# Optimization experiments

Measured on AMD Instinct MI355X. Metric: run time of the kernel, lower is better.

Reference implementation:

```python
import jax, jax.numpy as jnp
import numpy as np

B, T = 64, 128
IN, H, L, OUT = 512, 1024, 2, 1


def _gru_scan(seq, Wi, Wh, bi, bh):
    # seq: (S, in_dim); PyTorch GRU cell, gate order r, z, n.
    h0 = jnp.zeros((H,), dtype=seq.dtype)
    def step(h, x):
        gi = x @ Wi.T + bi          # (3H,)
        gh = h @ Wh.T + bh          # (3H,)
        r = jax.nn.sigmoid(gi[:H] + gh[:H])
        z = jax.nn.sigmoid(gi[H:2 * H] + gh[H:2 * H])
        n = jnp.tanh(gi[2 * H:] + r * gh[2 * H:])
        h_new = (1.0 - z) * n + z * h
        return h_new, h_new
    _, hs = jax.lax.scan(step, h0, seq)
    return hs                        # (S, H)


def setup_inputs() -> dict:
    key = jax.random.key(0)
    ks = jax.random.split(key, 24)
    mk = lambda k, shape: jax.random.normal(k, shape, dtype=jnp.float32) * 0.05
    d = {}
    d['x'] = jax.random.normal(ks[0], (B, T, IN), dtype=jnp.float32)
    # gru1: layer0 input=IN, layer1 input=H
    d['g1_Wi0'] = mk(ks[1], (3 * H, IN)); d['g1_Wh0'] = mk(ks[2], (3 * H, H))
    d['g1_bi0'] = mk(ks[3], (3 * H,));    d['g1_bh0'] = mk(ks[4], (3 * H,))
    d['g1_Wi1'] = mk(ks[5], (3 * H, H));  d['g1_Wh1'] = mk(ks[6], (3 * H, H))
    d['g1_bi1'] = mk(ks[7], (3 * H,));    d['g1_bh1'] = mk(ks[8], (3 * H,))
    # gru2: both layers input=H
    d['g2_Wi0'] = mk(ks[9], (3 * H, H));  d['g2_Wh0'] = mk(ks[10], (3 * H, H))
    d['g2_bi0'] = mk(ks[11], (3 * H,));   d['g2_bh0'] = mk(ks[12], (3 * H,))
    d['g2_Wi1'] = mk(ks[13], (3 * H, H)); d['g2_Wh1'] = mk(ks[14], (3 * H, H))
    d['g2_bi1'] = mk(ks[15], (3 * H,));   d['g2_bh1'] = mk(ks[16], (3 * H,))
    d['fc1_W'] = mk(ks[17], (64, H));     d['fc1_b'] = mk(ks[18], (64,))
    d['fc2_W'] = mk(ks[19], (OUT, 64));   d['fc2_b'] = mk(ks[20], (OUT,))
    return d


def reference(x, g1_Wi0, g1_Wh0, g1_bi0, g1_bh0, g1_Wi1, g1_Wh1, g1_bi1, g1_bh1,
              g2_Wi0, g2_Wh0, g2_bi0, g2_bh0, g2_Wi1, g2_Wh1, g2_bi1, g2_bh1,
              fc1_W, fc1_b, fc2_W, fc2_b):
    # PyTorch feeds x[:, t, :] (2-D) to a batch_first GRU -> treated as an
    # UNBATCHED sequence of length B; hidden is carried across t. That equals
    # one GRU scan over the flattened (T*B)-step sequence, t-major / b-minor.
    seq = jnp.swapaxes(x, 0, 1).reshape(T * B, IN)
    hs0 = _gru_scan(seq, g1_Wi0, g1_Wh0, g1_bi0, g1_bh0)    # (T*B, H) layer 0
    hs1 = _gru_scan(hs0, g1_Wi1, g1_Wh1, g1_bi1, g1_bh1)    # (T*B, H) layer 1
    # h returned after timestep t is the hidden at flat step t*B + (B-1)
    s = jnp.stack([hs0, hs1], axis=1)[B - 1::B]             # (T, L, H)
    seq2 = s.reshape(T * L, H)                              # torch.cat(s)
    # gru2 over the [1, T*L, H] sequence (batch=1)
    hs2_0 = _gru_scan(seq2, g2_Wi0, g2_Wh0, g2_bi0, g2_bh0)
    hs2_1 = _gru_scan(hs2_0, g2_Wi1, g2_Wh1, g2_bi1, g2_bh1)
    h2 = jnp.stack([hs2_0[-1], hs2_1[-1]], axis=0)[:, None, :]  # (L, 1, H)
    y = jax.nn.sigmoid(h2 @ fc1_W.T + fc1_b)                # (L, 1, 64)
    out = jax.nn.sigmoid(y @ fc2_W.T + fc2_b)               # (L, 1, OUT)
    return out
```

## Files before the change

### kernel.cpp

```cpp
#include <hip/hip_runtime.h>


typedef unsigned u32x4 __attribute__((ext_vector_type(4)));
typedef unsigned u32x2 __attribute__((ext_vector_type(2)));
typedef _Float16 h2_t  __attribute__((ext_vector_type(2)));

#define NWG 256

__device__ u32x4    g_recL0[2][NWG];
__device__ u32x4    g_recL1[2][NWG];
__device__ unsigned g_seq2[256][512];

__device__ __forceinline__ unsigned pk(float a, float b) {
  unsigned short ua = __builtin_bit_cast(unsigned short, (_Float16)a);
  unsigned short ub = __builtin_bit_cast(unsigned short, (_Float16)b);
  return (unsigned)ua | ((unsigned)ub << 16);
}
__device__ __forceinline__ float unpk(unsigned u, int hi) {
  unsigned short us = (unsigned short)(hi ? (u >> 16) : (u & 0xffffu));
  return (float)__builtin_bit_cast(_Float16, us);
}

#if __has_builtin(__builtin_amdgcn_fdot2)
__device__ __forceinline__ float fdot2(unsigned a, unsigned b, float c) {
  return __builtin_amdgcn_fdot2(__builtin_bit_cast(h2_t, a),
                                __builtin_bit_cast(h2_t, b), c, false);
}
#else
__device__ __forceinline__ float fdot2(unsigned a, unsigned b, float c) {
  h2_t ha = __builtin_bit_cast(h2_t, a), hb = __builtin_bit_cast(h2_t, b);
  return c + (float)ha[0] * (float)hb[0] + (float)ha[1] * (float)hb[1];
}
#endif

__device__ __forceinline__ u32x4 ld_sc_v4(const u32x4* p) {
  u32x4 v;
  asm volatile("global_load_dwordx4 %0, %1, off sc1\n\t"
               "s_waitcnt vmcnt(0)"
               : "=&v"(v) : "v"(p) : "memory");
  return v;
}
__device__ __forceinline__ void st_sc_v4(u32x4* p, u32x4 v) {
  asm volatile("global_store_dwordx4 %0, %1, off sc1"
               :: "v"(p), "v"(v) : "memory");
}
__device__ __forceinline__ void st_sc_v2(void* p, u32x2 v) {
  asm volatile("global_store_dwordx2 %0, %1, off sc1"
               :: "v"(p), "v"(v) : "memory");
}

__device__ __forceinline__ float rcpf(float x) {
#if __has_builtin(__builtin_amdgcn_rcpf)
  return __builtin_amdgcn_rcpf(x);
#else
  return 1.f / x;
#endif
}
__device__ __forceinline__ float sigf(float x) {
  return rcpf(1.f + __expf(-x));
}
__device__ __forceinline__ float tanh_f(float x) {
  x = fminf(fmaxf(x, -15.f), 15.f);
  const float e = __expf(2.f * x);
  return (e - 1.f) * rcpf(e + 1.f);
}

__device__ __forceinline__ int swzHc(int ch) { return ch ^ ((ch >> 3) & 7); }
__device__ __forceinline__ int swzXc(int ch) { return ch ^ ((ch >> 2) & 7); }
__device__ __forceinline__ int swzH_pos(int idx) { return (swzHc(idx >> 2) << 2) | (idx & 3); }
__device__ __forceinline__ int swzX_pos(int idx) { return (swzXc(idx >> 2) << 2) | (idx & 3); }

__global__ void init_recs() {
  int t = blockIdx.x * blockDim.x + threadIdx.x;
  u32x4 ff = {0u, 0u, 0xFFFFFFFFu, 0u};
  if (t < 512)       g_recL0[t >> 8][t & 255] = ff;
  else               g_recL1[(t - 512) >> 8][t & 255] = ff;
}

template <int PHASE>
__global__ __launch_bounds__(512, 2) void gru_phase(
    const float* __restrict__ Wm0, const float* __restrict__ Wm1,
    const float* __restrict__ Wm2, const float* __restrict__ Wm3,
    const float* __restrict__ bh0, const float* __restrict__ bi1,
    const float* __restrict__ bh1, const float* __restrict__ bi0,
    const float* __restrict__ x,
    const float* __restrict__ fc1W, const float* __restrict__ fc1b,
    const float* __restrict__ fc2W, const float* __restrict__ fc2b,
    float* __restrict__ out)
{
  constexpr int N0 = (PHASE == 1) ? 8192 : 256;
  constexpr int XC = (PHASE == 1) ? 512 : 1024;

  const int wg   = blockIdx.x;
  const int tid  = threadIdx.x;
  const int wv   = tid >> 6;
  const int lane = tid & 63;
  const int m    = wv >> 1;
  const int kh   = wv & 1;
  const int g4   = lane >> 4;
  const int q    = lane & 15;
  const int j0   = wg * 4;
  const bool m3s = (PHASE == 1) && (m == 3);

  __shared__ __attribute__((aligned(16))) unsigned sH0[2][512];
  __shared__ __attribute__((aligned(16))) unsigned sH1[2][512];
  __shared__ __attribute__((aligned(16))) unsigned sX [2][512];
  __shared__ float sD[2][96];
  __shared__ float sY[128];

  unsigned wreg[48];
  {
    const float* Wm = (m == 0) ? Wm0 : (m == 1) ? Wm1 : (m == 2) ? Wm2 : Wm3;
    const int cols = (m == 3) ? XC : 1024;
    #pragma unroll
    for (int t = 0; t < 3; ++t) {
      const int rr = g4 * 3 + t;
      const int R  = (rr >> 2) * 1024 + j0 + (rr & 3);
      const float2* rp = (const float2*)(Wm + (size_t)R * cols + kh * (cols / 2) + q * (cols / 32));
      if (m3s) {
        #pragma unroll
        for (int p = 0; p < 8; ++p)  { float2 v = rp[p]; wreg[t * 8 + p]  = pk(v.x, v.y); }
      } else {
        #pragma unroll
        for (int p = 0; p < 16; ++p) { float2 v = rp[p]; wreg[t * 16 + p] = pk(v.x, v.y); }
      }
    }
  }

  float bI[3], bH[3];
  {
    const int i = lane & 3, layer = (lane >> 2) & 1;
    const float* pbi = layer ? bi1 : bi0;
    const float* pbh = layer ? bh1 : bh0;
    #pragma unroll
    for (int g = 0; g < 3; ++g) {
      bI[g] = pbi[g * 1024 + j0 + i];
      bH[g] = pbh[g * 1024 + j0 + i];
    }
  }

  for (int s = 0; s <= N0; ++s) {
    const int par = s & 1;

    float2 xv = {0.f, 0.f};
    unsigned xs = 0;
    if (PHASE == 1) {
      if (s < N0 && tid < 256) {
        const int b = s & 63, tt = s >> 6;
        xv = ((const float2*)(x + (size_t)(b * 128 + tt) * 512))[tid];
      }
    } else {
      if (s < N0) xs = g_seq2[s][tid];
    }

    const int t2 = tid & 255;
    {
      unsigned d0 = 0, d1 = 0;
      if (s > 0) {
        const unsigned want = (unsigned)(s - 1);
        const u32x4* a = (tid < 256) ? &g_recL0[(s - 1) & 1][t2]
                                     : &g_recL1[(s - 1) & 1][t2];
        u32x4 r = ld_sc_v4(a);
        while (r[2] != want) {
          __builtin_amdgcn_s_sleep(1);
          r = ld_sc_v4(a);
        }
        d0 = r[0]; d1 = r[1];
      }
      unsigned* dst = (tid < 256) ? sH0[par] : sH1[par];
      dst[swzH_pos(2 * t2)]     = d0;
      dst[swzH_pos(2 * t2 + 1)] = d1;
    }
    if (PHASE == 1) {
      if (s < N0 && tid < 256) sX[par][swzX_pos(tid)] = pk(xv.x, xv.y);
    } else {
      if (s < N0) sX[par][swzH_pos(tid)] = xs;
    }
    __syncthreads();

    float acc0 = 0.f, acc1 = 0.f, acc2 = 0.f;
    if (m3s) {
      const u32x4* Xv = (const u32x4*)sX[par];
      #pragma unroll
      for (int k = 0; k < 2; ++k) {
        u32x4 h4 = Xv[swzXc(kh * 32 + 2 * q + k)];
        #pragma unroll
        for (int u = 0; u < 4; ++u) {
          const int p = 4 * k + u;
          acc0 = fdot2(wreg[p],      h4[u], acc0);
          acc1 = fdot2(wreg[8 + p],  h4[u], acc1);
          acc2 = fdot2(wreg[16 + p], h4[u], acc2);
        }
      }
    } else {
      const unsigned* hb = (m == 2) ? sH1[par] : (m == 3) ? sX[par] : sH0[par];
      const u32x4* Hv = (const u32x4*)hb;
      #pragma unroll
      for (int k = 0; k < 4; ++k) {
        u32x4 h4 = Hv[swzHc(kh * 64 + 4 * q + k)];
        #pragma unroll
        for (int u = 0; u < 4; ++u) {
          const int p = 4 * k + u;
          acc0 = fdot2(wreg[p],      h4[u], acc0);
          acc1 = fdot2(wreg[16 + p], h4[u], acc1);
          acc2 = fdot2(wreg[32 + p], h4[u], acc2);
        }
      }
    }
    acc0 += __shfl_xor(acc0, 8, 16); acc0 += __shfl_xor(acc0, 4, 16);
    acc0 += __shfl_xor(acc0, 2, 16); acc0 += __shfl_xor(acc0, 1, 16);
    acc1 += __shfl_xor(acc1, 8, 16); acc1 += __shfl_xor(acc1, 4, 16);
    acc1 += __shfl_xor(acc1, 2, 16); acc1 += __shfl_xor(acc1, 1, 16);
    acc2 += __shfl_xor(acc2, 8, 16); acc2 += __shfl_xor(acc2, 4, 16);
    acc2 += __shfl_xor(acc2, 2, 16); acc2 += __shfl_xor(acc2, 1, 16);
    if (q < 3) {
      const float dv = (q == 0) ? acc0 : (q == 1) ? acc1 : acc2;
      sD[par][m * 24 + kh * 12 + g4 * 3 + q] = dv;
    }
    __syncthreads();

    if (wv == 0) {
      const int i = lane & 3;
      const int layer = (lane >> 2) & 1;
      const float* Sd = sD[par];
      const int mI = layer ? 1 : 3;
      const int mH = layer ? 2 : 0;
      const float dIr = Sd[mI * 24 + 0 + i] + Sd[mI * 24 + 12 + 0 + i];
      const float dIz = Sd[mI * 24 + 4 + i] + Sd[mI * 24 + 12 + 4 + i];
      const float dIn = Sd[mI * 24 + 8 + i] + Sd[mI * 24 + 12 + 8 + i];
      const float dHr = Sd[mH * 24 + 0 + i] + Sd[mH * 24 + 12 + 0 + i];
      const float dHz = Sd[mH * 24 + 4 + i] + Sd[mH * 24 + 12 + 4 + i];
      const float dHn = Sd[mH * 24 + 8 + i] + Sd[mH * 24 + 12 + 8 + i];
      const float rg = sigf(dIr + bI[0] + dHr + bH[0]);
      const float zg = sigf(dIz + bI[1] + dHz + bH[1]);
      const float ng = tanh_f(dIn + bI[2] + rg * (dHn + bH[2]));
      const int   jj = 2 * wg + (i >> 1);
      const unsigned hu = (layer ? sH1 : sH0)[par][swzH_pos(jj)];
      const float hp = unpk(hu, i & 1);
      float hn = (1.f - zg) * ng + zg * hp;
      const bool valid = layer ? (s >= 1) : (s < N0);
      hn = valid ? hn : 0.f;
      const float v0 = __shfl(hn, 0), v1 = __shfl(hn, 1);
      const float v2 = __shfl(hn, 2), v3 = __shfl(hn, 3);
      const float w0 = __shfl(hn, 4), w1 = __shfl(hn, 5);
      const float w2 = __shfl(hn, 6), w3 = __shfl(hn, 7);
      if (lane == 0) {
        u32x4 rec0 = {pk(v0, v1), pk(v2, v3), (unsigned)s, 0u};
        u32x4 rec1 = {pk(w0, w1), pk(w2, w3), (unsigned)s, 0u};
        st_sc_v4(&g_recL0[par][wg], rec0);
        st_sc_v4(&g_recL1[par][wg], rec1);
        if (PHASE == 1) {
          if ((s & 63) == 63) {
            u32x2 t2v = {rec0[0], rec0[1]};
            st_sc_v2(&g_seq2[2 * (s >> 6)][2 * wg], t2v);
          }
          if (s >= 1 && ((s - 1) & 63) == 63) {
            u32x2 t2v = {rec1[0], rec1[1]};
            st_sc_v2(&g_seq2[2 * ((s - 1) >> 6) + 1][2 * wg], t2v);
          }
        }
      }
    }
  }

  if (PHASE == 2 && wg == 0) {
    if (tid < 256) {
      const u32x4* a1 = &g_recL1[0][tid];
      u32x4 r1 = ld_sc_v4(a1);
      while (r1[2] != 256u) { __builtin_amdgcn_s_sleep(1); r1 = ld_sc_v4(a1); }
      sH1[0][swzH_pos(2 * tid)]     = r1[0];
      sH1[0][swzH_pos(2 * tid + 1)] = r1[1];
    }
    __syncthreads();
    if (tid < 128) {
      const int lsel = tid >> 6;
      const int k = tid & 63;
      const unsigned* Hs = lsel ? sH1[0] : sH0[0];
      const float* wrow = fc1W + (size_t)k * 1024;
      float a = fc1b[k];
      for (int j2 = 0; j2 < 512; ++j2) {
        const unsigned hu = Hs[swzH_pos(j2)];
        a += unpk(hu, 0) * wrow[2 * j2] + unpk(hu, 1) * wrow[2 * j2 + 1];
      }
      sY[tid] = sigf(a);
    }
    __syncthreads();
    if (tid < 2) {
      const float* yv = sY + tid * 64;
      float a = fc2b[0];
      for (int k2 = 0; k2 < 64; ++k2) a += fc2W[k2] * yv[k2];
      out[tid] = sigf(a);
    }
  }
}

extern "C" void kernel_launch(void* const* d_in, const int* in_sizes, int n_in,
                              void* d_out, int out_size, void* d_ws, size_t ws_size,
                              hipStream_t stream) {
  (void)in_sizes; (void)n_in; (void)out_size; (void)d_ws; (void)ws_size;
  const float* x      = (const float*)d_in[0];
  const float* g1_Wi0 = (const float*)d_in[1];
  const float* g1_Wh0 = (const float*)d_in[2];
  const float* g1_bi0 = (const float*)d_in[3];
  const float* g1_bh0 = (const float*)d_in[4];
  const float* g1_Wi1 = (const float*)d_in[5];
  const float* g1_Wh1 = (const float*)d_in[6];
  const float* g1_bi1 = (const float*)d_in[7];
  const float* g1_bh1 = (const float*)d_in[8];
  const float* g2_Wi0 = (const float*)d_in[9];
  const float* g2_Wh0 = (const float*)d_in[10];
  const float* g2_bi0 = (const float*)d_in[11];
  const float* g2_bh0 = (const float*)d_in[12];
  const float* g2_Wi1 = (const float*)d_in[13];
  const float* g2_Wh1 = (const float*)d_in[14];
  const float* g2_bi1 = (const float*)d_in[15];
  const float* g2_bh1 = (const float*)d_in[16];
  const float* fc1W   = (const float*)d_in[17];
  const float* fc1b   = (const float*)d_in[18];
  const float* fc2W   = (const float*)d_in[19];
  const float* fc2b   = (const float*)d_in[20];
  float* out = (float*)d_out;

  init_recs<<<dim3(4), dim3(256), 0, stream>>>();
  gru_phase<1><<<dim3(NWG), dim3(512), 0, stream>>>(
      g1_Wh0, g1_Wi1, g1_Wh1, g1_Wi0, g1_bh0, g1_bi1, g1_bh1, g1_bi0,
      x, fc1W, fc1b, fc2W, fc2b, out);
  gru_phase<2><<<dim3(NWG), dim3(512), 0, stream>>>(
      g2_Wh0, g2_Wi1, g2_Wh1, g2_Wi0, g2_bh0, g2_bi1, g2_bh1, g2_bi0,
      x, fc1W, fc1b, fc2W, fc2b, out);
}
```

Measured before the change: 26.79 ms.

## Pipeline all four GRU layers in one persistent kernel with per-XCC roles

Replaces the two-phase launch, where each phase ran its two layers in lockstep, with a single persistent kernel. Workgroups claim slots through atomics and become one of four layer roles, each role placed on its own XCC when possible, so all four GRU layers run as a wavefront pipeline. Each layer's hidden states are written to full per-step history buffers with sequence tags, letting downstream layers prefetch inputs several steps ahead. Pollers on the same XCC spin mostly through L2 loads. This removes the serialization between the two GRU stacks, but adds a large init pass over the history buffers, relies on XCC_ID placement, and needs every workgroup co-resident to avoid deadlock.

After: 25.51 ms. -4.8%, faster.

```diff
diff --git a/kernel.cpp b/kernel.cpp
--- a/kernel.cpp
+++ b/kernel.cpp
@@ -2,14 +2,16 @@
 
 
 typedef unsigned u32x4 __attribute__((ext_vector_type(4)));
-typedef unsigned u32x2 __attribute__((ext_vector_type(2)));
 typedef _Float16 h2_t  __attribute__((ext_vector_type(2)));
 
-#define NWG 256
-
-__device__ u32x4    g_recL0[2][NWG];
-__device__ u32x4    g_recL1[2][NWG];
-__device__ unsigned g_seq2[256][512];
+#define S1 8192
+#define S2 256
+
+__device__ u32x4 g_h0s[S1][256];
+__device__ u32x4 g_h1s[S1][256];
+__device__ u32x4 g_q0s[S2][256];
+__device__ u32x4 g_q1s[S2][256];
+__device__ int   g_claim[128];
 
 __device__ __forceinline__ unsigned pk(float a, float b) {
   unsigned short ua = __builtin_bit_cast(unsigned short, (_Float16)a);
@@ -36,17 +38,17 @@
 __device__ __forceinline__ u32x4 ld_sc_v4(const u32x4* p) {
   u32x4 v;
   asm volatile("global_load_dwordx4 %0, %1, off sc1\n\t"
-               "s_waitcnt vmcnt(0)"
-               : "=&v"(v) : "v"(p) : "memory");
+               "s_waitcnt vmcnt(0)" : "=&v"(v) : "v"(p) : "memory");
   return v;
 }
+__device__ __forceinline__ u32x4 ld_l2_v4(const u32x4* p) {
+  u32x4 v;
+  asm volatile("global_load_dwordx4 %0, %1, off sc0\n\t"
+               "s_waitcnt vmcnt(0)" : "=&v"(v) : "v"(p) : "memory");
+  return v;
+}
 __device__ __forceinline__ void st_sc_v4(u32x4* p, u32x4 v) {
-  asm volatile("global_store_dwordx4 %0, %1, off sc1"
-               :: "v"(p), "v"(v) : "memory");
-}
-__device__ __forceinline__ void st_sc_v2(void* p, u32x2 v) {
-  asm volatile("global_store_dwordx2 %0, %1, off sc1"
-               :: "v"(p), "v"(v) : "memory");
+  asm volatile("global_store_dwordx4 %0, %1, off sc1" :: "v"(p), "v"(v) : "memory");
 }
 
 __device__ __forceinline__ float rcpf(float x) {
@@ -56,9 +58,7 @@
   return 1.f / x;
 #endif
 }
-__device__ __forceinline__ float sigf(float x) {
-  return rcpf(1.f + __expf(-x));
-}
+__device__ __forceinline__ float sigf(float x) { return rcpf(1.f + __expf(-x)); }
 __device__ __forceinline__ float tanh_f(float x) {
   x = fminf(fmaxf(x, -15.f), 15.f);
   const float e = __expf(2.f * x);
@@ -66,230 +66,309 @@
 }
 
 __device__ __forceinline__ int swzHc(int ch) { return ch ^ ((ch >> 3) & 7); }
+__device__ __forceinline__ int swzH_pos(int i) { return (swzHc(i >> 2) << 2) | (i & 3); }
 __device__ __forceinline__ int swzXc(int ch) { return ch ^ ((ch >> 2) & 7); }
-__device__ __forceinline__ int swzH_pos(int idx) { return (swzHc(idx >> 2) << 2) | (idx & 3); }
-__device__ __forceinline__ int swzX_pos(int idx) { return (swzXc(idx >> 2) << 2) | (idx & 3); }
-
-__global__ void init_recs() {
-  int t = blockIdx.x * blockDim.x + threadIdx.x;
-  u32x4 ff = {0u, 0u, 0xFFFFFFFFu, 0u};
-  if (t < 512)       g_recL0[t >> 8][t & 255] = ff;
-  else               g_recL1[(t - 512) >> 8][t & 255] = ff;
-}
-
-template <int PHASE>
-__global__ __launch_bounds__(512, 2) void gru_phase(
-    const float* __restrict__ Wm0, const float* __restrict__ Wm1,
-    const float* __restrict__ Wm2, const float* __restrict__ Wm3,
-    const float* __restrict__ bh0, const float* __restrict__ bi1,
-    const float* __restrict__ bh1, const float* __restrict__ bi0,
-    const float* __restrict__ x,
-    const float* __restrict__ fc1W, const float* __restrict__ fc1b,
-    const float* __restrict__ fc2W, const float* __restrict__ fc2b,
-    float* __restrict__ out)
+__device__ __forceinline__ int swzX_pos(int i) { return (swzXc(i >> 2) << 2) | (i & 3); }
+
+__global__ void init_all() {
+  const long long NH = (long long)S1 * 256;
+  const long long NQ = (long long)S2 * 256;
+  const long long N  = 2 * NH + 2 * NQ;
+  for (long long k = (long long)blockIdx.x * blockDim.x + threadIdx.x; k < N;
+       k += (long long)gridDim.x * blockDim.x) {
+    u32x4* r;
+    long long k2 = k;
+    if (k2 < NH) r = &g_h0s[0][0] + k2;
+    else {
+      k2 -= NH;
+      if (k2 < NH) r = &g_h1s[0][0] + k2;
+      else {
+        k2 -= NH;
+        if (k2 < NQ) r = &g_q0s[0][0] + k2;
+        else         r = &g_q1s[0][0] + (k2 - NQ);
+      }
+    }
+    (*r)[2] = 0xFFFFFFFFu;
+  }
+  if (blockIdx.x == 0 && threadIdx.x < 128) g_claim[threadIdx.x] = 0;
+}
+
+__device__ __forceinline__ const u32x4* in_addr(int role, int u, int r) {
+  if (role == 1) return &g_h0s[u][r];
+  if (role == 2) {
+    const int ss = ((u >> 1) << 6) + 63;
+    return (u & 1) ? &g_h1s[ss][r] : &g_h0s[ss][r];
+  }
+  return &g_q0s[u][r];
+}
+__device__ __forceinline__ unsigned in_want(int role, int u) {
+  return (role == 2) ? (unsigned)(((u >> 1) << 6) + 63) : (unsigned)u;
+}
+
+#define MAC4(A, W4, H4)                                                       \
+  A = fdot2((W4)[0], (H4)[0], A); A = fdot2((W4)[1], (H4)[1], A);             \
+  A = fdot2((W4)[2], (H4)[2], A); A = fdot2((W4)[3], (H4)[3], A);
+
+#define RED16(A)                                                              \
+  A += __shfl_xor(A, 8, 16); A += __shfl_xor(A, 4, 16);                       \
+  A += __shfl_xor(A, 2, 16); A += __shfl_xor(A, 1, 16);
+
+__global__
+__attribute__((amdgpu_flat_work_group_size(512, 512), amdgpu_waves_per_eu(2, 2)))
+void gru_all(const float* __restrict__ x,
+             const float* __restrict__ g1_Wi0, const float* __restrict__ g1_Wh0,
+             const float* __restrict__ g1_bi0, const float* __restrict__ g1_bh0,
+             const float* __restrict__ g1_Wi1, const float* __restrict__ g1_Wh1,
+             const float* __restrict__ g1_bi1, const float* __restrict__ g1_bh1,
+             const float* __restrict__ g2_Wi0, const float* __restrict__ g2_Wh0,
+             const float* __restrict__ g2_bi0, const float* __restrict__ g2_bh0,
+             const float* __restrict__ g2_Wi1, const float* __restrict__ g2_Wh1,
+             const float* __restrict__ g2_bi1, const float* __restrict__ g2_bh1,
+             const float* __restrict__ fc1W, const float* __restrict__ fc1b,
+             const float* __restrict__ fc2W, const float* __restrict__ fc2b,
+             float* __restrict__ out)
 {
-  constexpr int N0 = (PHASE == 1) ? 8192 : 256;
-  constexpr int XC = (PHASE == 1) ? 512 : 1024;
-
-  const int wg   = blockIdx.x;
-  const int tid  = threadIdx.x;
-  const int wv   = tid >> 6;
-  const int lane = tid & 63;
-  const int m    = wv >> 1;
-  const int kh   = wv & 1;
-  const int g4   = lane >> 4;
-  const int q    = lane & 15;
-  const int j0   = wg * 4;
-  const bool m3s = (PHASE == 1) && (m == 3);
-
-  __shared__ __attribute__((aligned(16))) unsigned sH0[2][512];
-  __shared__ __attribute__((aligned(16))) unsigned sH1[2][512];
-  __shared__ __attribute__((aligned(16))) unsigned sX [2][512];
-  __shared__ float sD[2][96];
+  const int tid = threadIdx.x;
+  const int G   = tid >> 4;
+  const int q   = tid & 15;
+  const int rid = tid - 256;
+
+  __shared__ __attribute__((aligned(16))) unsigned sH[2][512];
+  __shared__ __attribute__((aligned(16))) unsigned sIN[8][512];
+  __shared__ __attribute__((aligned(16))) unsigned sX[8][256];
+  __shared__ float sD[96];
+  __shared__ float sDI[96];
   __shared__ float sY[128];
-
-  unsigned wreg[48];
+  __shared__ int   sSlot;
+
+  unsigned xcc;
+  asm volatile("s_getreg_b32 %0, hwreg(HW_REG_XCC_ID)" : "=s"(xcc));
+  xcc &= 7u;
+  if (tid == 0) {
+    int slot = -1;
+    if (xcc < 4u) {
+      for (int i = 0; i < 32 && slot < 0; ++i)
+        if (atomicCAS(&g_claim[(int)xcc * 32 + i], 0, 1) == 0)
+          slot = (int)xcc * 32 + i;
+    }
+    if (slot < 0) {
+      for (int k = 0; k < 32; ++k) __builtin_amdgcn_s_sleep(64);
+      for (int i = 0; i < 128 && slot < 0; ++i)
+        if (atomicCAS(&g_claim[i], 0, 1) == 0) slot = i;
+    }
+    sSlot = slot;
+  }
+  __syncthreads();
+  const int slot = sSlot;
+  if (slot < 0) return;
+  const int role = slot >> 5;
+  const int rank = slot & 31;
+  const int e0   = rank * 32;
+  const bool lp  = ((int)xcc == role);
+  const int S    = (role <= 1) ? S1 : S2;
+
+  const float* Wh  = (role == 0) ? g1_Wh0 : (role == 1) ? g1_Wh1
+                   : (role == 2) ? g2_Wh0 : g2_Wh1;
+  const float* Wi  = (role == 0) ? g1_Wi0 : (role == 1) ? g1_Wi1
+                   : (role == 2) ? g2_Wi0 : g2_Wi1;
+  const float* pbi = (role == 0) ? g1_bi0 : (role == 1) ? g1_bi1
+                   : (role == 2) ? g2_bi0 : g2_bi1;
+  const float* pbh = (role == 0) ? g1_bh0 : (role == 1) ? g1_bh1
+                   : (role == 2) ? g2_bh0 : g2_bh1;
+  u32x4 (*outA)[256] = (role == 0) ? g_h0s : (role == 1) ? g_h1s
+                     : (role == 2) ? g_q0s : g_q1s;
+
+  u32x4 wv[6][8];
   {
-    const float* Wm = (m == 0) ? Wm0 : (m == 1) ? Wm1 : (m == 2) ? Wm2 : Wm3;
-    const int cols = (m == 3) ? XC : 1024;
+    const bool isWh = (G < 16);
+    const int  Gm   = isWh ? G : (G - 16);
+    const float* M  = isWh ? Wh : Wi;
+    const bool wide = isWh || (role != 0);
     #pragma unroll
-    for (int t = 0; t < 3; ++t) {
-      const int rr = g4 * 3 + t;
-      const int R  = (rr >> 2) * 1024 + j0 + (rr & 3);
-      const float2* rp = (const float2*)(Wm + (size_t)R * cols + kh * (cols / 2) + q * (cols / 32));
-      if (m3s) {
+    for (int j = 0; j < 6; ++j) {
+      const int rr = Gm * 6 + j;
+      const int R  = (rr >> 5) * 1024 + e0 + (rr & 31);
+      if (wide) {
+        const float4* rp = (const float4*)(M + (size_t)R * 1024 + 64 * q);
         #pragma unroll
-        for (int p = 0; p < 8; ++p)  { float2 v = rp[p]; wreg[t * 8 + p]  = pk(v.x, v.y); }
+        for (int c = 0; c < 8; ++c) {
+          float4 a = rp[2 * c], b = rp[2 * c + 1];
+          wv[j][c] = (u32x4){pk(a.x, a.y), pk(a.z, a.w), pk(b.x, b.y), pk(b.z, b.w)};
+        }
+      } else {
+        const float4* rp = (const float4*)(M + (size_t)R * 512 + 32 * q);
+        #pragma unroll
+        for (int c = 0; c < 4; ++c) {
+          float4 a = rp[2 * c], b = rp[2 * c + 1];
+          wv[j][c] = (u32x4){pk(a.x, a.y), pk(a.z, a.w), pk(b.x, b.y), pk(b.z, b.w)};
+        }
+      }
+    }
+  }
+
+  float bIr = 0, bIz = 0, bIn = 0, bHr = 0, bHz = 0, bHn = 0;
+  if (tid < 32) {
+    const int ge = e0 + tid;
+    bIr = pbi[ge]; bIz = pbi[1024 + ge]; bIn = pbi[2048 + ge];
+    bHr = pbh[ge]; bHz = pbh[1024 + ge]; bHn = pbh[2048 + ge];
+  }
+
+  if (tid >= 256) {
+    if (role == 0) {
+      #pragma unroll
+      for (int u = 0; u < 4; ++u) {
+        float2 xv = ((const float2*)(x + (size_t)((u & 63) * 128 + (u >> 6)) * 512))[rid];
+        sX[u][swzX_pos(rid)] = pk(xv.x, xv.y);
+      }
+    } else {
+      for (int u = 0; u < 4; ++u) {
+        const u32x4* a = in_addr(role, u, rid);
+        const unsigned w = in_want(role, u);
+        u32x4 r = ld_sc_v4(a);
+        while (r[2] != w) r = ld_sc_v4(a);
+        sIN[u][swzH_pos(2 * rid)]     = r[0];
+        sIN[u][swzH_pos(2 * rid + 1)] = r[1];
+      }
+    }
+  }
+  __syncthreads();
+
+  for (int s = 0; s < S; ++s) {
+    const int par = s & 1;
+
+    if (tid >= 256 && (s & 3) == 0) {
+      if (role == 0) {
+        #pragma unroll
+        for (int k = 0; k < 4; ++k) {
+          const int u = s + 4 + k;
+          if (u < S) {
+            float2 xv = ((const float2*)(x + (size_t)((u & 63) * 128 + (u >> 6)) * 512))[rid];
+            sX[u & 7][swzX_pos(rid)] = pk(xv.x, xv.y);
+          }
+        }
       } else {
         #pragma unroll
-        for (int p = 0; p < 16; ++p) { float2 v = rp[p]; wreg[t * 16 + p] = pk(v.x, v.y); }
-      }
-    }
-  }
-
-  float bI[3], bH[3];
-  {
-    const int i = lane & 3, layer = (lane >> 2) & 1;
-    const float* pbi = layer ? bi1 : bi0;
-    const float* pbh = layer ? bh1 : bh0;
-    #pragma unroll
-    for (int g = 0; g < 3; ++g) {
-      bI[g] = pbi[g * 1024 + j0 + i];
-      bH[g] = pbh[g * 1024 + j0 + i];
-    }
-  }
-
-  for (int s = 0; s <= N0; ++s) {
-    const int par = s & 1;
-
-    float2 xv = {0.f, 0.f};
-    unsigned xs = 0;
-    if (PHASE == 1) {
-      if (s < N0 && tid < 256) {
-        const int b = s & 63, tt = s >> 6;
-        xv = ((const float2*)(x + (size_t)(b * 128 + tt) * 512))[tid];
-      }
-    } else {
-      if (s < N0) xs = g_seq2[s][tid];
-    }
-
-    const int t2 = tid & 255;
-    {
+        for (int k = 0; k < 4; ++k) {
+          const int u = s + 4 + k;
+          if (u < S) {
+            const u32x4* a = in_addr(role, u, rid);
+            const unsigned w = in_want(role, u);
+            u32x4 r = ld_sc_v4(a);
+            while (r[2] != w) r = ld_sc_v4(a);
+            sIN[u & 7][swzH_pos(2 * rid)]     = r[0];
+            sIN[u & 7][swzH_pos(2 * rid + 1)] = r[1];
+          }
+        }
+      }
+    }
+
+    if (tid < 256) {
       unsigned d0 = 0, d1 = 0;
       if (s > 0) {
-        const unsigned want = (unsigned)(s - 1);
-        const u32x4* a = (tid < 256) ? &g_recL0[(s - 1) & 1][t2]
-                                     : &g_recL1[(s - 1) & 1][t2];
-        u32x4 r = ld_sc_v4(a);
-        while (r[2] != want) {
-          __builtin_amdgcn_s_sleep(1);
+        const unsigned w = (unsigned)(s - 1);
+        const u32x4* a = &outA[s - 1][tid];
+        u32x4 r;
+        if (lp) {
+          r = ld_l2_v4(a);
+          int spin = 0;
+          while (r[2] != w)
+            r = (((++spin) & 7) == 0) ? ld_sc_v4(a) : ld_l2_v4(a);
+        } else {
           r = ld_sc_v4(a);
+          while (r[2] != w) r = ld_sc_v4(a);
         }
         d0 = r[0]; d1 = r[1];
       }
-      unsigned* dst = (tid < 256) ? sH0[par] : sH1[par];
-      dst[swzH_pos(2 * t2)]     = d0;
-      dst[swzH_pos(2 * t2 + 1)] = d1;
-    }
-    if (PHASE == 1) {
-      if (s < N0 && tid < 256) sX[par][swzX_pos(tid)] = pk(xv.x, xv.y);
+      sH[par][swzH_pos(2 * tid)]     = d0;
+      sH[par][swzH_pos(2 * tid + 1)] = d1;
+    }
+    __syncthreads();
+
+    float a0 = 0, a1 = 0, a2 = 0, a3 = 0, a4 = 0, a5 = 0;
+    if (G < 16) {
+      const u32x4* HV = (const u32x4*)sH[par];
+      #pragma unroll
+      for (int c = 0; c < 8; ++c) {
+        const u32x4 h4 = HV[8 * q + (c ^ (q & 7))];
+        MAC4(a0, wv[0][c], h4); MAC4(a1, wv[1][c], h4); MAC4(a2, wv[2][c], h4);
+        MAC4(a3, wv[3][c], h4); MAC4(a4, wv[4][c], h4); MAC4(a5, wv[5][c], h4);
+      }
+    } else if (role != 0) {
+      const u32x4* IV = (const u32x4*)sIN[s & 7];
+      #pragma unroll
+      for (int c = 0; c < 8; ++c) {
+        const u32x4 h4 = IV[8 * q + (c ^ (q & 7))];
+        MAC4(a0, wv[0][c], h4); MAC4(a1, wv[1][c], h4); MAC4(a2, wv[2][c], h4);
+        MAC4(a3, wv[3][c], h4); MAC4(a4, wv[4][c], h4); MAC4(a5, wv[5][c], h4);
+      }
     } else {
-      if (s < N0) sX[par][swzH_pos(tid)] = xs;
+      const u32x4* XV = (const u32x4*)sX[s & 7];
+      #pragma unroll
+      for (int c = 0; c < 4; ++c) {
+        const int ch = 4 * q + c;
+        const u32x4 h4 = XV[ch ^ ((ch >> 2) & 7)];
+        MAC4(a0, wv[0][c], h4); MAC4(a1, wv[1][c], h4); MAC4(a2, wv[2][c], h4);
+        MAC4(a3, wv[3][c], h4); MAC4(a4, wv[4][c], h4); MAC4(a5, wv[5][c], h4);
+      }
+    }
+    RED16(a0); RED16(a1); RED16(a2); RED16(a3); RED16(a4); RED16(a5);
+    if (q < 6) {
+      const float v = (q == 0) ? a0 : (q == 1) ? a1 : (q == 2) ? a2
+                    : (q == 3) ? a3 : (q == 4) ? a4 : a5;
+      if (G < 16) sD[G * 6 + q] = v;
+      else        sDI[(G - 16) * 6 + q] = v;
     }
     __syncthreads();
 
-    float acc0 = 0.f, acc1 = 0.f, acc2 = 0.f;
-    if (m3s) {
-      const u32x4* Xv = (const u32x4*)sX[par];
-      #pragma unroll
-      for (int k = 0; k < 2; ++k) {
-        u32x4 h4 = Xv[swzXc(kh * 32 + 2 * q + k)];
-        #pragma unroll
-        for (int u = 0; u < 4; ++u) {
-          const int p = 4 * k + u;
-          acc0 = fdot2(wreg[p],      h4[u], acc0);
-          acc1 = fdot2(wreg[8 + p],  h4[u], acc1);
-          acc2 = fdot2(wreg[16 + p], h4[u], acc2);
-        }
-      }
+    if (tid < 32) {
+      const float rg = sigf(sDI[tid] + bIr + sD[tid] + bHr);
+      const float zg = sigf(sDI[32 + tid] + bIz + sD[32 + tid] + bHz);
+      const float ng = tanh_f(sDI[64 + tid] + bIn + rg * (sD[64 + tid] + bHn));
+      const int ge = e0 + tid;
+      const float hp = unpk(sH[par][swzH_pos(ge >> 1)], ge & 1);
+      const float hn = (1.f - zg) * ng + zg * hp;
+      const int b4 = (tid & 7) * 4;
+      const float v0 = __shfl(hn, b4),     v1 = __shfl(hn, b4 + 1);
+      const float v2 = __shfl(hn, b4 + 2), v3 = __shfl(hn, b4 + 3);
+      if (tid < 8) {
+        u32x4 rec = {pk(v0, v1), pk(v2, v3), (unsigned)s, 0u};
+        st_sc_v4(&outA[s][rank * 8 + tid], rec);
+      }
+    }
+  }
+
+  if (role == 3 && rank == 0) {
+    if (tid < 256) {
+      const u32x4* a = &g_q0s[S2 - 1][tid];
+      u32x4 r = ld_sc_v4(a);
+      while (r[2] != (unsigned)(S2 - 1)) r = ld_sc_v4(a);
+      sH[0][swzH_pos(2 * tid)]     = r[0];
+      sH[0][swzH_pos(2 * tid + 1)] = r[1];
     } else {
-      const unsigned* hb = (m == 2) ? sH1[par] : (m == 3) ? sX[par] : sH0[par];
-      const u32x4* Hv = (const u32x4*)hb;
-      #pragma unroll
-      for (int k = 0; k < 4; ++k) {
-        u32x4 h4 = Hv[swzHc(kh * 64 + 4 * q + k)];
-        #pragma unroll
-        for (int u = 0; u < 4; ++u) {
-          const int p = 4 * k + u;
-          acc0 = fdot2(wreg[p],      h4[u], acc0);
-          acc1 = fdot2(wreg[16 + p], h4[u], acc1);
-          acc2 = fdot2(wreg[32 + p], h4[u], acc2);
-        }
-      }
-    }
-    acc0 += __shfl_xor(acc0, 8, 16); acc0 += __shfl_xor(acc0, 4, 16);
-    acc0 += __shfl_xor(acc0, 2, 16); acc0 += __shfl_xor(acc0, 1, 16);
-    acc1 += __shfl_xor(acc1, 8, 16); acc1 += __shfl_xor(acc1, 4, 16);
-    acc1 += __shfl_xor(acc1, 2, 16); acc1 += __shfl_xor(acc1, 1, 16);
-    acc2 += __shfl_xor(acc2, 8, 16); acc2 += __shfl_xor(acc2, 4, 16);
-    acc2 += __shfl_xor(acc2, 2, 16); acc2 += __shfl_xor(acc2, 1, 16);
-    if (q < 3) {
-      const float dv = (q == 0) ? acc0 : (q == 1) ? acc1 : acc2;
-      sD[par][m * 24 + kh * 12 + g4 * 3 + q] = dv;
-    }
-    __syncthreads();
-
-    if (wv == 0) {
-      const int i = lane & 3;
-      const int layer = (lane >> 2) & 1;
-      const float* Sd = sD[par];
-      const int mI = layer ? 1 : 3;
-      const int mH = layer ? 2 : 0;
-      const float dIr = Sd[mI * 24 + 0 + i] + Sd[mI * 24 + 12 + 0 + i];
-      const float dIz = Sd[mI * 24 + 4 + i] + Sd[mI * 24 + 12 + 4 + i];
-      const float dIn = Sd[mI * 24 + 8 + i] + Sd[mI * 24 + 12 + 8 + i];
-      const float dHr = Sd[mH * 24 + 0 + i] + Sd[mH * 24 + 12 + 0 + i];
-      const float dHz = Sd[mH * 24 + 4 + i] + Sd[mH * 24 + 12 + 4 + i];
-      const float dHn = Sd[mH * 24 + 8 + i] + Sd[mH * 24 + 12 + 8 + i];
-      const float rg = sigf(dIr + bI[0] + dHr + bH[0]);
-      const float zg = sigf(dIz + bI[1] + dHz + bH[1]);
-      const float ng = tanh_f(dIn + bI[2] + rg * (dHn + bH[2]));
-      const int   jj = 2 * wg + (i >> 1);
-      const unsigned hu = (layer ? sH1 : sH0)[par][swzH_pos(jj)];
-      const float hp = unpk(hu, i & 1);
-      float hn = (1.f - zg) * ng + zg * hp;
-      const bool valid = layer ? (s >= 1) : (s < N0);
-      hn = valid ? hn : 0.f;
-      const float v0 = __shfl(hn, 0), v1 = __shfl(hn, 1);
-      const float v2 = __shfl(hn, 2), v3 = __shfl(hn, 3);
-      const float w0 = __shfl(hn, 4), w1 = __shfl(hn, 5);
-      const float w2 = __shfl(hn, 6), w3 = __shfl(hn, 7);
-      if (lane == 0) {
-        u32x4 rec0 = {pk(v0, v1), pk(v2, v3), (unsigned)s, 0u};
-        u32x4 rec1 = {pk(w0, w1), pk(w2, w3), (unsigned)s, 0u};
-        st_sc_v4(&g_recL0[par][wg], rec0);
-        st_sc_v4(&g_recL1[par][wg], rec1);
-        if (PHASE == 1) {
-          if ((s & 63) == 63) {
-            u32x2 t2v = {rec0[0], rec0[1]};
-            st_sc_v2(&g_seq2[2 * (s >> 6)][2 * wg], t2v);
-          }
-          if (s >= 1 && ((s - 1) & 63) == 63) {
-            u32x2 t2v = {rec1[0], rec1[1]};
-            st_sc_v2(&g_seq2[2 * ((s - 1) >> 6) + 1][2 * wg], t2v);
-          }
-        }
-      }
-    }
-  }
-
-  if (PHASE == 2 && wg == 0) {
-    if (tid < 256) {
-      const u32x4* a1 = &g_recL1[0][tid];
-      u32x4 r1 = ld_sc_v4(a1);
-      while (r1[2] != 256u) { __builtin_amdgcn_s_sleep(1); r1 = ld_sc_v4(a1); }
-      sH1[0][swzH_pos(2 * tid)]     = r1[0];
-      sH1[0][swzH_pos(2 * tid + 1)] = r1[1];
+      const u32x4* a = &g_q1s[S2 - 1][rid];
+      u32x4 r = ld_sc_v4(a);
+      while (r[2] != (unsigned)(S2 - 1)) r = ld_sc_v4(a);
+      sH[1][swzH_pos(2 * rid)]     = r[0];
+      sH[1][swzH_pos(2 * rid + 1)] = r[1];
     }
     __syncthreads();
     if (tid < 128) {
-      const int lsel = tid >> 6;
-      const int k = tid & 63;
-      const unsigned* Hs = lsel ? sH1[0] : sH0[0];
+      const int l = tid >> 6, k = tid & 63;
+      const unsigned* Hs = (const unsigned*)sH[l];
       const float* wrow = fc1W + (size_t)k * 1024;
-      float a = fc1b[k];
+      float acc = fc1b[k];
       for (int j2 = 0; j2 < 512; ++j2) {
         const unsigned hu = Hs[swzH_pos(j2)];
-        a += unpk(hu, 0) * wrow[2 * j2] + unpk(hu, 1) * wrow[2 * j2 + 1];
-      }
-      sY[tid] = sigf(a);
+        acc += unpk(hu, 0) * wrow[2 * j2] + unpk(hu, 1) * wrow[2 * j2 + 1];
+      }
+      sY[tid] = sigf(acc);
     }
     __syncthreads();
     if (tid < 2) {
       const float* yv = sY + tid * 64;
-      float a = fc2b[0];
-      for (int k2 = 0; k2 < 64; ++k2) a += fc2W[k2] * yv[k2];
-      out[tid] = sigf(a);
+      float acc = fc2b[0];
+      for (int k2 = 0; k2 < 64; ++k2) acc += fc2W[k2] * yv[k2];
+      out[tid] = sigf(acc);
     }
   }
 }
@@ -321,11 +400,9 @@
   const float* fc2b   = (const float*)d_in[20];
   float* out = (float*)d_out;
 
-  init_recs<<<dim3(4), dim3(256), 0, stream>>>();
-  gru_phase<1><<<dim3(NWG), dim3(512), 0, stream>>>(
-      g1_Wh0, g1_Wi1, g1_Wh1, g1_Wi0, g1_bh0, g1_bi1, g1_bh1, g1_bi0,
-      x, fc1W, fc1b, fc2W, fc2b, out);
-  gru_phase<2><<<dim3(NWG), dim3(512), 0, stream>>>(
-      g2_Wh0, g2_Wi1, g2_Wh1, g2_Wi0, g2_bh0, g2_bi1, g2_bh1, g2_bi0,
-      x, fc1W, fc1b, fc2W, fc2b, out);
-}
+  init_all<<<dim3(2048), dim3(256), 0, stream>>>();
+  gru_all<<<dim3(256), dim3(512), 0, stream>>>(
+      x, g1_Wi0, g1_Wh0, g1_bi0, g1_bh0, g1_Wi1, g1_Wh1, g1_bi1, g1_bh1,
+      g2_Wi0, g2_Wh0, g2_bi0, g2_bh0, g2_Wi1, g2_Wh1, g2_bi1, g2_bh1,
+      fc1W, fc1b, fc2W, fc2b, out);
+}
```
